# Performance work log

Hardware: AMD Instinct MI355X
Metric: run time of the kernel (lower is better)

## Reference

```python
import jax, jax.numpy as jnp
import numpy as np

B, HG, WG = 2, 64, 64
N = HG * WG
C_IN, C_HID, HEADS, C_OUT = 512, 256, 4, 512
NEG_SLOPE = 0.2   # PyG GATv2Conv default negative_slope
LN_EPS = 1e-5


def _grid_edges(h, w):
    """8-neighborhood grid graph, edge_index[0]=source, edge_index[1]=target."""
    nodes = np.arange(h * w).reshape(h, w)
    srcs, dsts = [], []
    for dh in (-1, 0, 1):
        for dw in (-1, 0, 1):
            if dh == 0 and dw == 0:
                continue
            r0, r1 = max(0, -dh), h - max(0, dh)
            c0, c1 = max(0, -dw), w - max(0, dw)
            srcs.append(nodes[r0:r1, c0:c1].ravel())
            dsts.append(nodes[r0 + dh:r1 + dh, c0 + dw:c1 + dw].ravel())
    return np.stack([np.concatenate(srcs), np.concatenate(dsts)]).astype(np.int64)


def setup_inputs() -> dict:
    key = jax.random.key(0)
    ks = iter(jax.random.split(key, 32))

    def p(shape, scale=0.02):
        return jax.random.normal(next(ks), shape, dtype=jnp.float32) * scale

    return {
        "rgb_features": jax.random.normal(next(ks), (B, N, C_IN), dtype=jnp.float32),
        "x_features": jax.random.normal(next(ks), (B, N, C_IN), dtype=jnp.float32),
        "edge_index": jnp.asarray(_grid_edges(HG, WG)),
        # modality_fusion: Linear(2*C_IN, C_HID) + LayerNorm
        "fusion_w": p((C_HID, 2 * C_IN)), "fusion_b": jnp.zeros((C_HID,), jnp.float32),
        "fusion_g": jnp.ones((C_HID,), jnp.float32), "fusion_beta": jnp.zeros((C_HID,), jnp.float32),
        # GATSegmentation.in_proj + norm
        "inproj_w": p((C_HID, C_HID)), "inproj_b": jnp.zeros((C_HID,), jnp.float32),
        "norm_g": jnp.ones((C_HID,), jnp.float32), "norm_b": jnp.zeros((C_HID,), jnp.float32),
        # GATv2Conv layer 0: C_HID -> C_HID, heads=4, concat=True
        "l0_wl": p((HEADS * C_HID, C_HID)), "l0_bl": jnp.zeros((HEADS * C_HID,), jnp.float32),
        "l0_wr": p((HEADS * C_HID, C_HID)), "l0_br": jnp.zeros((HEADS * C_HID,), jnp.float32),
        "l0_att": p((HEADS, C_HID)), "l0_bias": jnp.zeros((HEADS * C_HID,), jnp.float32),
        # GATv2Conv layer 1 (final): 4*C_HID -> C_HID, heads=1, concat=False
        "l1_wl": p((C_HID, HEADS * C_HID)), "l1_bl": jnp.zeros((C_HID,), jnp.float32),
        "l1_wr": p((C_HID, HEADS * C_HID)), "l1_br": jnp.zeros((C_HID,), jnp.float32),
        "l1_att": p((1, C_HID)), "l1_bias": jnp.zeros((C_HID,), jnp.float32),
        # final_proj: 1x1 conv C_HID -> C_OUT
        "fp_w": p((C_OUT, C_HID)), "fp_b": jnp.zeros((C_OUT,), jnp.float32),
    }


def _ln(x, g, b):
    mu = x.mean(-1, keepdims=True)
    v = ((x - mu) ** 2).mean(-1, keepdims=True)
    return (x - mu) * jax.lax.rsqrt(v + LN_EPS) * g + b


def _gatv2(x, src, dst, wl, bl, wr, br, att, bias, concat):
    """PyG GATv2Conv (share_weights=False): gather, leaky_relu logit, segment softmax over
    target neighborhoods, scatter-add aggregation."""
    n = x.shape[0]
    heads, c = att.shape
    xl = (x @ wl.T + bl).reshape(n, heads, c)   # source-side transform (x_j)
    xr = (x @ wr.T + br).reshape(n, heads, c)   # target-side transform (x_i)
    e = jax.nn.leaky_relu(xl[src] + xr[dst], NEG_SLOPE)        # [E, H, C]
    logit = jnp.einsum('ehc,hc->eh', e, att)                   # [E, H]
    m = jax.ops.segment_max(logit, dst, num_segments=n)
    p = jnp.exp(logit - m[dst])
    z = jax.ops.segment_sum(p, dst, num_segments=n)
    alpha = p / z[dst]                                          # softmax per target node
    out = jax.ops.segment_sum(xl[src] * alpha[..., None], dst, num_segments=n)  # [N, H, C]
    out = out.reshape(n, heads * c) if concat else out.mean(axis=1)
    return out + bias


def reference(rgb_features, x_features, edge_index, fusion_w, fusion_b, fusion_g, fusion_beta,
              inproj_w, inproj_b, norm_g, norm_b,
              l0_wl, l0_bl, l0_wr, l0_br, l0_att, l0_bias,
              l1_wl, l1_bl, l1_wr, l1_br, l1_att, l1_bias,
              fp_w, fp_b):
    b, n, _ = rgb_features.shape
    loops = jnp.arange(n, dtype=edge_index.dtype)  # PyG add_self_loops=True
    src = jnp.concatenate([edge_index[0], loops])
    dst = jnp.concatenate([edge_index[1], loops])

    def single(rgb, xm):  # one graph in the batch (original loops over B in Python)
        comb = jnp.concatenate([rgb, xm], axis=-1)                     # [N, 2*C_IN]
        f = jax.nn.relu(_ln(comb @ fusion_w.T + fusion_b, fusion_g, fusion_beta))
        h = jax.nn.relu(_ln(f @ inproj_w.T + inproj_b, norm_g, norm_b))
        h = jax.nn.relu(_gatv2(h, src, dst, l0_wl, l0_bl, l0_wr, l0_br, l0_att, l0_bias, True))
        h = jax.nn.relu(_gatv2(h, src, dst, l1_wl, l1_bl, l1_wr, l1_br, l1_att, l1_bias, False))
        return h                                                        # [N, C_HID]

    nodes = jax.vmap(single)(rgb_features, x_features)                  # [B, N, C_HID]
    img = nodes.reshape(b, HG, WG, C_HID)
    return jnp.einsum('bhwc,oc->bohw', img, fp_w) + fp_b[None, :, None, None]
```

## Files before the change

kernel.cpp:

```cpp
#include <hip/hip_runtime.h>


#define NNODE 4096
#define LN_EPS 1e-5f
#define LOG2E 1.4426950408889634f

typedef _Float16 half8 __attribute__((ext_vector_type(8)));
typedef _Float16 half4 __attribute__((ext_vector_type(4)));
typedef _Float16 h2 __attribute__((ext_vector_type(2)));
typedef float f32x4 __attribute__((ext_vector_type(4)));

__device__ __forceinline__ float wave_reduce_sum(float v) {
    #pragma unroll
    for (int off = 32; off > 0; off >>= 1) v += __shfl_xor(v, off, 64);
    return v;
}

__device__ __forceinline__ void gload_lds16(const void* g, void* l) {
    __builtin_amdgcn_global_load_lds(
        (const __attribute__((address_space(1))) void*)g,
        (__attribute__((address_space(3))) void*)l, 16, 0, 0);
}

template<int N> __device__ __forceinline__ void waitcnt_vm() {
    if constexpr (N <= 0)      asm volatile("s_waitcnt vmcnt(0)" ::: "memory");
    else if constexpr (N == 2) asm volatile("s_waitcnt vmcnt(2)" ::: "memory");
    else if constexpr (N == 3) asm volatile("s_waitcnt vmcnt(3)" ::: "memory");
    else if constexpr (N == 4) asm volatile("s_waitcnt vmcnt(4)" ::: "memory");
    else                       asm volatile("s_waitcnt vmcnt(8)" ::: "memory");
}
template<int N> __device__ __forceinline__ void waitcnt_vm_lgkm() {
    if constexpr (N <= 0)      asm volatile("s_waitcnt vmcnt(0) lgkmcnt(0)" ::: "memory");
    else if constexpr (N == 2) asm volatile("s_waitcnt vmcnt(2) lgkmcnt(0)" ::: "memory");
    else if constexpr (N == 3) asm volatile("s_waitcnt vmcnt(3) lgkmcnt(0)" ::: "memory");
    else                       asm volatile("s_waitcnt vmcnt(4) lgkmcnt(0)" ::: "memory");
}
__device__ __forceinline__ void barrier_raw() {
    asm volatile("s_barrier" ::: "memory");
}

__device__ __forceinline__ int xcd_swz(int lin, int total) {
    return (lin & 7) * (total >> 3) + (lin >> 3);
}

template<int IT, int JT, int OUTMODE>
__global__ __launch_bounds__(256) void gemm3_k(
    const _Float16* __restrict__ A, const _Float16* __restrict__ W,
    const float* __restrict__ bias_lo, const float* __restrict__ bias_hi,
    int nsplit, void* __restrict__ Cout, int K, int N)
{
    constexpr int BM = 32 * IT, BN = 32 * JT;
    constexpr int CA = (BM * 4) / 256;
    constexpr int CB = (BN * 4) / 256;
    constexpr int L = CA + CB;
    __shared__ _Float16 ldsA[3][BM * 32];
    __shared__ _Float16 ldsB[3][BN * 32];

    const int tid = threadIdx.x;
    const int lin = blockIdx.y * gridDim.x + blockIdx.x;
    const int swz = xcd_swz(lin, gridDim.x * gridDim.y);
    const int m0 = (swz / gridDim.x) * BM, n0 = (swz % gridDim.x) * BN;
    const int lane = tid & 63, w = tid >> 6;
    const int fr = lane & 15, kq = lane >> 4;
    const int sq = (kq ^ (fr & 3)) * 8;
    const int wm = (w & 1) * (16 * IT), wn = (w >> 1) * (16 * JT);

    const _Float16* aP[CA]; int aC[CA];
    #pragma unroll
    for (int i = 0; i < CA; ++i) {
        const int c = i * 256 + tid, r = c >> 2, q = (c & 3) ^ (r & 3);
        aP[i] = A + (size_t)(m0 + r) * K + q * 8;
        aC[i] = c * 8;
    }
    const _Float16* bP[CB]; int bC[CB];
    #pragma unroll
    for (int i = 0; i < CB; ++i) {
        const int c = i * 256 + tid, r = c >> 2, q = (c & 3) ^ (r & 3);
        bP[i] = W + (size_t)(n0 + r) * K + q * 8;
        bC[i] = c * 8;
    }

    f32x4 acc[IT][JT] = {};
    const int NT = K >> 5;

    #pragma unroll
    for (int i = 0; i < CA; ++i) gload_lds16(aP[i], &ldsA[0][aC[i]]);
    #pragma unroll
    for (int i = 0; i < CB; ++i) gload_lds16(bP[i], &ldsB[0][bC[i]]);
    #pragma unroll
    for (int i = 0; i < CA; ++i) gload_lds16(aP[i] + 32, &ldsA[1][aC[i]]);
    #pragma unroll
    for (int i = 0; i < CB; ++i) gload_lds16(bP[i] + 32, &ldsB[1][bC[i]]);

    int bi = 0;
    for (int t = 0; t < NT; ++t) {
        if (t + 1 < NT) waitcnt_vm<L>(); else waitcnt_vm<0>();
        barrier_raw();
        if (t + 2 < NT) {
            int nb = bi + 2; if (nb >= 3) nb -= 3;
            const int k2 = (t + 2) << 5;
            #pragma unroll
            for (int i = 0; i < CA; ++i) gload_lds16(aP[i] + k2, &ldsA[nb][aC[i]]);
            #pragma unroll
            for (int i = 0; i < CB; ++i) gload_lds16(bP[i] + k2, &ldsB[nb][bC[i]]);
        }
        half8 af[IT], bf[JT];
        #pragma unroll
        for (int i = 0; i < IT; ++i)
            af[i] = *(const half8*)&ldsA[bi][(wm + i * 16 + fr) * 32 + sq];
        #pragma unroll
        for (int j = 0; j < JT; ++j)
            bf[j] = *(const half8*)&ldsB[bi][(wn + j * 16 + fr) * 32 + sq];
        #pragma unroll
        for (int i = 0; i < IT; ++i)
            #pragma unroll
            for (int j = 0; j < JT; ++j) {
                if (OUTMODE == 1)
                    acc[i][j] = __builtin_amdgcn_mfma_f32_16x16x32_f16(
                        bf[j], af[i], acc[i][j], 0, 0, 0);
                else
                    acc[i][j] = __builtin_amdgcn_mfma_f32_16x16x32_f16(
                        af[i], bf[j], acc[i][j], 0, 0, 0);
            }
        ++bi; if (bi == 3) bi = 0;
    }

    if (OUTMODE == 1) {
        #pragma unroll
        for (int i = 0; i < IT; ++i) {
            const int m = m0 + wm + i * 16 + fr;
            #pragma unroll
            for (int j = 0; j < JT; ++j) {
                const int nb4 = n0 + wn + j * 16 + kq * 4;
                const float* bp = (nb4 < nsplit) ? bias_lo + nb4
                                                 : bias_hi + (nb4 - nsplit);
                const float4 bv = *(const float4*)bp;
                half4 ov = {(_Float16)(acc[i][j][0] + bv.x),
                            (_Float16)(acc[i][j][1] + bv.y),
                            (_Float16)(acc[i][j][2] + bv.z),
                            (_Float16)(acc[i][j][3] + bv.w)};
                *(half4*)((_Float16*)Cout + (size_t)m * N + nb4) = ov;
            }
        }
    } else {
        #pragma unroll
        for (int j = 0; j < JT; ++j) {
            const int col = n0 + wn + j * 16 + fr;
            const float bc = (col < nsplit) ? bias_lo[col] : bias_hi[col - nsplit];
            #pragma unroll
            for (int i = 0; i < IT; ++i) {
                const int mrun = m0 + wm + i * 16 + kq * 4;
                const int b = mrun >> 12, node = mrun & 4095;
                float4 ov = {acc[i][j][0] + bc, acc[i][j][1] + bc,
                             acc[i][j][2] + bc, acc[i][j][3] + bc};
                *(float4*)((float*)Cout + ((size_t)(b * N + col)) * 4096 + node) = ov;
            }
        }
    }
}

__global__ __launch_bounds__(512) void fusion2_k(
    const float* __restrict__ A0, const float* __restrict__ A1,
    const _Float16* __restrict__ W1, const float* __restrict__ b1,
    const float* __restrict__ g1, const float* __restrict__ be1,
    const _Float16* __restrict__ W2, const float* __restrict__ b2,
    const float* __restrict__ g2, const float* __restrict__ be2,
    _Float16* __restrict__ out)
{
    __shared__ _Float16 lA[3][32 * 32];
    __shared__ _Float16 lB[3][256 * 32];
    __shared__ float lC[32 * 260];
    __shared__ _Float16 lH[8 * 1024];

    const int tid = threadIdx.x;
    const int m0 = blockIdx.x * 32;
    const int lane = tid & 63, w = tid >> 6;
    const int fr = lane & 15, kq = lane >> 4;
    const int sq = (kq ^ (fr & 3)) * 8;
    const int wr = (w & 1) * 16, wc = (w >> 1) * 64;
    const bool stager = (tid < 128);

    const _Float16* bP[2]; int bC[2];
    #pragma unroll
    for (int i = 0; i < 2; ++i) {
        const int c = i * 512 + tid, r = c >> 2, q = (c & 3) ^ (r & 3);
        bP[i] = W1 + (size_t)r * 1024 + q * 8;
        bC[i] = c * 8;
    }
    const int ar = tid >> 2, aq = tid & 3;
    const int asw = (ar * 4 + (aq ^ (ar & 3))) * 8;
    float4 p0, p1;
    auto loadA = [&](int k) {
        const int gk = k + aq * 8;
        const float* s = (gk < 512) ? A0 + (size_t)(m0 + ar) * 512 + gk
                                    : A1 + (size_t)(m0 + ar) * 512 + gk - 512;
        p0 = *(const float4*)s;
        p1 = *(const float4*)(s + 4);
    };
    auto writeA = [&](int b) {
        half8 hv = {(_Float16)p0.x, (_Float16)p0.y, (_Float16)p0.z, (_Float16)p0.w,
                    (_Float16)p1.x, (_Float16)p1.y, (_Float16)p1.z, (_Float16)p1.w};
        *(half8*)&lA[b][asw] = hv;
    };

    f32x4 acc[4] = {};

    if (stager) { loadA(0); writeA(0); loadA(32); }
    #pragma unroll
    for (int i = 0; i < 2; ++i) gload_lds16(bP[i], &lB[0][bC[i]]);
    #pragma unroll
    for (int i = 0; i < 2; ++i) gload_lds16(bP[i] + 32, &lB[1][bC[i]]);

    int bi = 0;
    for (int t = 0; t < 32; ++t) {
        if (t + 1 < 32) {
            if (stager) waitcnt_vm_lgkm<4>(); else waitcnt_vm_lgkm<2>();
        } else {
            waitcnt_vm_lgkm<0>();
        }
        barrier_raw();
        int nb1 = bi + 1; if (nb1 >= 3) nb1 -= 3;
        int nb2 = bi + 2; if (nb2 >= 3) nb2 -= 3;
        if (stager && t + 1 < 32) writeA(nb1);
        if (t + 2 < 32) {
            const int k2 = (t + 2) << 5;
            if (stager) loadA(k2);
            #pragma unroll
            for (int i = 0; i < 2; ++i) gload_lds16(bP[i] + k2, &lB[nb2][bC[i]]);
        }
        half8 af = *(const half8*)&lA[bi][(wr + fr) * 32 + sq];
        half8 bf[4];
        #pragma unroll
        for (int j = 0; j < 4; ++j)
            bf[j] = *(const half8*)&lB[bi][(wc + j * 16 + fr) * 32 + sq];
        #pragma unroll
        for (int j = 0; j < 4; ++j)
            acc[j] = __builtin_amdgcn_mfma_f32_16x16x32_f16(af, bf[j], acc[j], 0, 0, 0);
        ++bi; if (bi == 3) bi = 0;
    }

    #pragma unroll
    for (int j = 0; j < 4; ++j) {
        const int col = wc + j * 16 + fr;
        const float bc = b1[col];
        #pragma unroll
        for (int r4 = 0; r4 < 4; ++r4)
            lC[(wr + kq * 4 + r4) * 260 + col] = acc[j][r4] + bc;
    }
    __syncthreads();

    {
        const float4 gv = *(const float4*)(g1 + lane * 4);
        const float4 bv = *(const float4*)(be1 + lane * 4);
        const int t2i = lane >> 3, gq = (lane >> 1) & 3, qo = (lane & 1) * 4;
        #pragma unroll
        for (int rr = 0; rr < 4; ++rr) {
            const int row = w * 4 + rr;
            const float4 v = *(const float4*)&lC[row * 260 + lane * 4];
            float s  = v.x + v.y + v.z + v.w;
            float s2 = v.x * v.x + v.y * v.y + v.z * v.z + v.w * v.w;
            s = wave_reduce_sum(s);
            s2 = wave_reduce_sum(s2);
            const float mu  = s * (1.0f / 256.0f);
            const float var = s2 * (1.0f / 256.0f) - mu * mu;
            const float rs  = rsqrtf(var + LN_EPS);
            half4 o;
            o[0] = (_Float16)fmaxf((v.x - mu) * rs * gv.x + bv.x, 0.f);
            o[1] = (_Float16)fmaxf((v.y - mu) * rs * gv.y + bv.y, 0.f);
            o[2] = (_Float16)fmaxf((v.z - mu) * rs * gv.z + bv.z, 0.f);
            o[3] = (_Float16)fmaxf((v.w - mu) * rs * gv.w + bv.w, 0.f);
            const int qslot = gq ^ (row & 3);
            *(half4*)&lH[t2i * 1024 + (row * 4 + qslot) * 8 + qo] = o;
        }
    }
    __syncthreads();

    const _Float16* b2P[2]; int b2C[2];
    #pragma unroll
    for (int i = 0; i < 2; ++i) {
        const int c = i * 512 + tid, r = c >> 2, q = (c & 3) ^ (r & 3);
        b2P[i] = W2 + (size_t)r * 256 + q * 8;
        b2C[i] = c * 8;
    }
    f32x4 acc2[4] = {};
    #pragma unroll
    for (int i = 0; i < 2; ++i) gload_lds16(b2P[i], &lB[0][b2C[i]]);
    #pragma unroll
    for (int i = 0; i < 2; ++i) gload_lds16(b2P[i] + 32, &lB[1][b2C[i]]);

    int bi2 = 0;
    for (int t2 = 0; t2 < 8; ++t2) {
        if (t2 + 1 < 8) waitcnt_vm<2>(); else waitcnt_vm<0>();
        barrier_raw();
        if (t2 + 2 < 8) {
            int nb = bi2 + 2; if (nb >= 3) nb -= 3;
            const int k2 = (t2 + 2) << 5;
            #pragma unroll
            for (int i = 0; i < 2; ++i) gload_lds16(b2P[i] + k2, &lB[nb][b2C[i]]);
        }
        const half8 af = *(const half8*)
            &lH[t2 * 1024 + ((wr + fr) * 4 + (kq ^ (fr & 3))) * 8];
        half8 bf[4];
        #pragma unroll
        for (int j = 0; j < 4; ++j)
            bf[j] = *(const half8*)&lB[bi2][(wc + j * 16 + fr) * 32 + sq];
        #pragma unroll
        for (int j = 0; j < 4; ++j)
            acc2[j] = __builtin_amdgcn_mfma_f32_16x16x32_f16(af, bf[j], acc2[j], 0, 0, 0);
        ++bi2; if (bi2 == 3) bi2 = 0;
    }

    #pragma unroll
    for (int j = 0; j < 4; ++j) {
        const int col = wc + j * 16 + fr;
        const float bc = b2[col];
        #pragma unroll
        for (int r4 = 0; r4 < 4; ++r4)
            lC[(wr + kq * 4 + r4) * 260 + col] = acc2[j][r4] + bc;
    }
    __syncthreads();

    {
        const float4 gv = *(const float4*)(g2 + lane * 4);
        const float4 bv = *(const float4*)(be2 + lane * 4);
        #pragma unroll
        for (int rr = 0; rr < 4; ++rr) {
            const int row = w * 4 + rr;
            const float4 v = *(const float4*)&lC[row * 260 + lane * 4];
            float s  = v.x + v.y + v.z + v.w;
            float s2 = v.x * v.x + v.y * v.y + v.z * v.z + v.w * v.w;
            s = wave_reduce_sum(s);
            s2 = wave_reduce_sum(s2);
            const float mu  = s * (1.0f / 256.0f);
            const float var = s2 * (1.0f / 256.0f) - mu * mu;
            const float rs  = rsqrtf(var + LN_EPS);
            half4 o;
            o[0] = (_Float16)fmaxf((v.x - mu) * rs * gv.x + bv.x, 0.f);
            o[1] = (_Float16)fmaxf((v.y - mu) * rs * gv.y + bv.y, 0.f);
            o[2] = (_Float16)fmaxf((v.z - mu) * rs * gv.z + bv.z, 0.f);
            o[3] = (_Float16)fmaxf((v.w - mu) * rs * gv.w + bv.w, 0.f);
            *(half4*)(out + (size_t)(m0 + row) * 256 + lane * 4) = o;
        }
    }
}

template<int HEADS, int LD, int XROFF, int OC>
__global__ __launch_bounds__(256) void gat4_k(
    const _Float16* __restrict__ xlr, const _Float16* __restrict__ att16,
    const float* __restrict__ bias, _Float16* __restrict__ out)
{
    const int tid = threadIdx.x, wv = tid >> 6, lane = tid & 63;
    const int g = lane >> 4, li = lane & 15;
    const int blk = xcd_swz(blockIdx.x, gridDim.x);
    const int wid = blk * 4 + wv;
    const int gi = (HEADS == 4) ? wid : wid * 4 + g;
    const int h  = (HEADS == 4) ? g : 0;
    const int node = gi & (NNODE - 1);
    const int base = gi - node;
    const int nr = node >> 6, nc = node & 63;
    const int co = h * 256 + li * 16;

    int sidx[9]; float msk[9];
    {
        const int drs[8] = {-1,-1,-1, 0, 0, 1, 1, 1};
        const int dcs[8] = {-1, 0, 1,-1, 1,-1, 0, 1};
        #pragma unroll
        for (int j = 0; j < 8; ++j) {
            const int rj = nr + drs[j], cj = nc + dcs[j];
            const bool v = ((unsigned)rj < 64u) & ((unsigned)cj < 64u);
            sidx[j] = v ? (rj * 64 + cj) : node;
            msk[j] = v ? 0.f : -1e30f;
        }
        sidx[8] = node; msk[8] = 0.f;
    }

    const _Float16* xp = xlr + (size_t)base * LD + co;

    half8 x0[9], x1[9];
    #pragma unroll
    for (int j = 0; j < 9; ++j) {
        x0[j] = *(const half8*)(xp + (size_t)sidx[j] * LD);
        x1[j] = *(const half8*)(xp + (size_t)sidx[j] * LD + 8);
    }
    const half8 xr0 = *(const half8*)(xlr + (size_t)gi * LD + XROFF + co);
    const half8 xr1 = *(const half8*)(xlr + (size_t)gi * LD + XROFF + co + 8);
    const half8 at0 = *(const half8*)(att16 + h * 256 + li * 16);
    const half8 at1 = *(const half8*)(att16 + h * 256 + li * 16 + 8);
    const h2 hz = {(_Float16)0.f, (_Float16)0.f};
    const h2 c02 = {(_Float16)0.2f, (_Float16)0.2f};

    float lg[9];
    #pragma unroll
    for (int j = 0; j < 9; ++j) {
        h2 p = hz;
        #pragma unroll
        for (int k = 0; k < 4; ++k) {
            h2 e = ((const h2*)&x0[j])[k] + ((const h2*)&xr0)[k];
            h2 tt = __builtin_elementwise_fma(
                __builtin_elementwise_min(e, hz), c02,
                __builtin_elementwise_max(e, hz));
            p = __builtin_elementwise_fma(tt, ((const h2*)&at0)[k], p);
        }
        #pragma unroll
        for (int k = 0; k < 4; ++k) {
            h2 e = ((const h2*)&x1[j])[k] + ((const h2*)&xr1)[k];
            h2 tt = __builtin_elementwise_fma(
                __builtin_elementwise_min(e, hz), c02,
                __builtin_elementwise_max(e, hz));
            p = __builtin_elementwise_fma(tt, ((const h2*)&at1)[k], p);
        }
        float pl = (float)p[0] + (float)p[1];
        pl += __shfl_xor(pl, 1, 64);
        pl += __shfl_xor(pl, 2, 64);
        pl += __shfl_xor(pl, 4, 64);
        pl += __shfl_xor(pl, 8, 64);
        lg[j] = pl + msk[j];
    }

    float m = lg[0];
    #pragma unroll
    for (int j = 1; j < 9; ++j) m = fmaxf(m, lg[j]);
    float pj[9], z = 0.f;
    #pragma unroll
    for (int j = 0; j < 9; ++j) { pj[j] = __builtin_amdgcn_exp2f(lg[j] - m); z += pj[j]; }
    const float inv = __builtin_amdgcn_rcpf(z);

    float acc[16];
    #pragma unroll
    for (int k = 0; k < 16; ++k) acc[k] = 0.f;
    #pragma unroll
    for (int j = 0; j < 9; ++j) {
        const float wj = pj[j];
        #pragma unroll
        for (int k = 0; k < 8; ++k) acc[k]     += wj * (float)x0[j][k];
        #pragma unroll
        for (int k = 0; k < 8; ++k) acc[8 + k] += wj * (float)x1[j][k];
    }
    float bv[16];
    #pragma unroll
    for (int q = 0; q < 4; ++q) {
        const float4 b4 = *(const float4*)(bias + h * 256 + li * 16 + q * 4);
        bv[q * 4 + 0] = b4.x; bv[q * 4 + 1] = b4.y;
        bv[q * 4 + 2] = b4.z; bv[q * 4 + 3] = b4.w;
    }
    half8 o0, o1;
    #pragma unroll
    for (int k = 0; k < 8; ++k) o0[k] = (_Float16)fmaxf(acc[k] * inv + bv[k], 0.f);
    #pragma unroll
    for (int k = 0; k < 8; ++k) o1[k] = (_Float16)fmaxf(acc[8 + k] * inv + bv[8 + k], 0.f);
    *(half8*)(out + (size_t)gi * OC + co) = o0;
    *(half8*)(out + (size_t)gi * OC + co + 8) = o1;
}

struct WTab {
    const float* src[9];
    int startblk[10];
    int nelem[9];
    int dstoff[9];
    float scale[9];
};

__global__ __launch_bounds__(256) void wconv_k(WTab t, _Float16* __restrict__ dst)
{
    const int b = blockIdx.x;
    int s = 0;
    #pragma unroll
    for (int i = 1; i < 9; ++i) s += (b >= t.startblk[i]);
    const int e0 = (b - t.startblk[s]) * 1024 + threadIdx.x * 4;
    if (e0 >= t.nelem[s]) return;
    const float4 v = *(const float4*)(t.src[s] + e0);
    const float sc = t.scale[s];
    half4 o = {(_Float16)(v.x * sc), (_Float16)(v.y * sc),
               (_Float16)(v.z * sc), (_Float16)(v.w * sc)};
    *(half4*)(dst + t.dstoff[s] + e0) = o;
}

extern "C" void kernel_launch(void* const* d_in, const int* in_sizes, int n_in,
                              void* d_out, int out_size, void* d_ws, size_t ws_size,
                              hipStream_t stream)
{
    const float* rgb       = (const float*)d_in[0];
    const float* xm        = (const float*)d_in[1];
    const float* fusion_w  = (const float*)d_in[3];
    const float* fusion_b  = (const float*)d_in[4];
    const float* fusion_g  = (const float*)d_in[5];
    const float* fusion_be = (const float*)d_in[6];
    const float* inproj_w  = (const float*)d_in[7];
    const float* inproj_b  = (const float*)d_in[8];
    const float* norm_g    = (const float*)d_in[9];
    const float* norm_b    = (const float*)d_in[10];
    const float* l0_wl     = (const float*)d_in[11];
    const float* l0_bl     = (const float*)d_in[12];
    const float* l0_wr     = (const float*)d_in[13];
    const float* l0_br     = (const float*)d_in[14];
    const float* l0_att    = (const float*)d_in[15];
    const float* l0_bias   = (const float*)d_in[16];
    const float* l1_wl     = (const float*)d_in[17];
    const float* l1_bl     = (const float*)d_in[18];
    const float* l1_wr     = (const float*)d_in[19];
    const float* l1_br     = (const float*)d_in[20];
    const float* l1_att    = (const float*)d_in[21];
    const float* l1_bias   = (const float*)d_in[22];
    const float* fp_w      = (const float*)d_in[23];
    const float* fp_b      = (const float*)d_in[24];

    char* ws = (char*)d_ws;
    _Float16* Wf16 = (_Float16*)ws;
    _Float16* H1   = (_Float16*)(ws + 4194304);
    _Float16* XLR0 = (_Float16*)(ws + 8388608);
    _Float16* GO0  = (_Float16*)(ws + 41943040);
    _Float16* XLR1 = (_Float16*)(ws + 58720256);
    _Float16* GO1  = (_Float16*)(ws + 67108864);

    _Float16* w_fus  = Wf16 + 0;
    _Float16* w_inp  = Wf16 + 262144;
    _Float16* w_l0   = Wf16 + 327680;
    _Float16* w_l1   = Wf16 + 851968;
    _Float16* w_fp   = Wf16 + 1376256;
    _Float16* att0_h = Wf16 + 1507328;
    _Float16* att1_h = Wf16 + 1508352;

    WTab t;
    const float* srcs[9] = {fusion_w, inproj_w, l0_wl, l0_wr, l1_wl, l1_wr,
                            fp_w, l0_att, l1_att};
    const int nel[9]  = {262144, 65536, 262144, 262144, 262144, 262144,
                         131072, 1024, 256};
    const int doff[9] = {0, 262144, 327680, 589824, 851968, 1114112,
                         1376256, 1507328, 1508352};
    const int sblk[10] = {0, 256, 320, 576, 832, 1088, 1344, 1472, 1473, 1474};
    for (int i = 0; i < 9; ++i) {
        t.src[i] = srcs[i]; t.nelem[i] = nel[i]; t.dstoff[i] = doff[i];
        t.scale[i] = (i >= 7) ? LOG2E : 1.0f;
    }
    for (int i = 0; i < 10; ++i) t.startblk[i] = sblk[i];

    wconv_k<<<1474, 256, 0, stream>>>(t, Wf16);

    fusion2_k<<<256, 512, 0, stream>>>(
        rgb, xm, w_fus, fusion_b, fusion_g, fusion_be,
        w_inp, inproj_b, norm_g, norm_b, H1);

    gemm3_k<4, 4, 1><<<dim3(16, 64), 256, 0, stream>>>(
        H1, w_l0, l0_bl, l0_br, 1024, XLR0, 256, 2048);

    gat4_k<4, 2048, 1024, 1024><<<2048, 256, 0, stream>>>(
        XLR0, att0_h, l0_bias, GO0);

    gemm3_k<2, 4, 1><<<dim3(4, 128), 256, 0, stream>>>(
        GO0, w_l1, l1_bl, l1_br, 256, XLR1, 1024, 512);

    gat4_k<1, 512, 256, 256><<<512, 256, 0, stream>>>(
        XLR1, att1_h, l1_bias, GO1);

    gemm3_k<2, 4, 2><<<dim3(4, 128), 256, 0, stream>>>(
        GO1, w_fp, fp_b, fp_b, 512, d_out, 256, 512);
}
```

Measured before the change: 116.8 us.

## Halve fusion2 row tile to 16 and use double-buffered pipeline

Fused fusion+inproj kernel now processes 16 rows per block instead of 32, doubling the grid to 512 blocks so more CUs are occupied. Each wave covers 32 output columns instead of a 16x64 sub-tile. The triple-buffered, counter-based pipeline is replaced by a simpler double buffer that waits on vmcnt(0) and a full __syncthreads each K step. The weight tiles are now reloaded by twice as many blocks, and the per-step full wait lets less load latency overlap with compute.

```diff
diff --git a/kernel.cpp b/kernel.cpp
--- a/kernel.cpp
+++ b/kernel.cpp
@@ -28,12 +28,6 @@
     else if constexpr (N == 3) asm volatile("s_waitcnt vmcnt(3)" ::: "memory");
     else if constexpr (N == 4) asm volatile("s_waitcnt vmcnt(4)" ::: "memory");
     else                       asm volatile("s_waitcnt vmcnt(8)" ::: "memory");
-}
-template<int N> __device__ __forceinline__ void waitcnt_vm_lgkm() {
-    if constexpr (N <= 0)      asm volatile("s_waitcnt vmcnt(0) lgkmcnt(0)" ::: "memory");
-    else if constexpr (N == 2) asm volatile("s_waitcnt vmcnt(2) lgkmcnt(0)" ::: "memory");
-    else if constexpr (N == 3) asm volatile("s_waitcnt vmcnt(3) lgkmcnt(0)" ::: "memory");
-    else                       asm volatile("s_waitcnt vmcnt(4) lgkmcnt(0)" ::: "memory");
 }
 __device__ __forceinline__ void barrier_raw() {
     asm volatile("s_barrier" ::: "memory");
@@ -167,18 +161,18 @@
     const float* __restrict__ g2, const float* __restrict__ be2,
     _Float16* __restrict__ out)
 {
-    __shared__ _Float16 lA[3][32 * 32];
-    __shared__ _Float16 lB[3][256 * 32];
-    __shared__ float lC[32 * 260];
-    __shared__ _Float16 lH[8 * 1024];
+    __shared__ _Float16 lA[2][16 * 32];
+    __shared__ _Float16 lB[2][256 * 32];
+    __shared__ float lC[16 * 260];
+    __shared__ _Float16 lH[8 * 512];
 
     const int tid = threadIdx.x;
-    const int m0 = blockIdx.x * 32;
+    const int m0 = blockIdx.x * 16;
     const int lane = tid & 63, w = tid >> 6;
     const int fr = lane & 15, kq = lane >> 4;
     const int sq = (kq ^ (fr & 3)) * 8;
-    const int wr = (w & 1) * 16, wc = (w >> 1) * 64;
-    const bool stager = (tid < 128);
+    const int wc = w * 32;
+    const bool stager = (tid < 64);
 
     const _Float16* bP[2]; int bC[2];
     #pragma unroll
@@ -203,49 +197,46 @@
         *(half8*)&lA[b][asw] = hv;
     };
 
-    f32x4 acc[4] = {};
-
-    if (stager) { loadA(0); writeA(0); loadA(32); }
+    f32x4 acc[2] = {};
+
+    if (stager) { loadA(0); writeA(0); }
     #pragma unroll
     for (int i = 0; i < 2; ++i) gload_lds16(bP[i], &lB[0][bC[i]]);
-    #pragma unroll
-    for (int i = 0; i < 2; ++i) gload_lds16(bP[i] + 32, &lB[1][bC[i]]);
-
-    int bi = 0;
+    asm volatile("s_waitcnt vmcnt(0)" ::: "memory");
+    __syncthreads();
+
+    int cur = 0;
     for (int t = 0; t < 32; ++t) {
-        if (t + 1 < 32) {
-            if (stager) waitcnt_vm_lgkm<4>(); else waitcnt_vm_lgkm<2>();
-        } else {
-            waitcnt_vm_lgkm<0>();
-        }
-        barrier_raw();
-        int nb1 = bi + 1; if (nb1 >= 3) nb1 -= 3;
-        int nb2 = bi + 2; if (nb2 >= 3) nb2 -= 3;
-        if (stager && t + 1 < 32) writeA(nb1);
-        if (t + 2 < 32) {
-            const int k2 = (t + 2) << 5;
-            if (stager) loadA(k2);
-            #pragma unroll
-            for (int i = 0; i < 2; ++i) gload_lds16(bP[i] + k2, &lB[nb2][bC[i]]);
-        }
-        half8 af = *(const half8*)&lA[bi][(wr + fr) * 32 + sq];
-        half8 bf[4];
-        #pragma unroll
-        for (int j = 0; j < 4; ++j)
-            bf[j] = *(const half8*)&lB[bi][(wc + j * 16 + fr) * 32 + sq];
-        #pragma unroll
-        for (int j = 0; j < 4; ++j)
+        const int pf = (t + 1 < 32);
+        if (pf) {
+            const int k1 = (t + 1) << 5;
+            if (stager) loadA(k1);
+            #pragma unroll
+            for (int i = 0; i < 2; ++i) gload_lds16(bP[i] + k1, &lB[cur ^ 1][bC[i]]);
+        }
+        const half8 af = *(const half8*)&lA[cur][fr * 32 + sq];
+        half8 bf[2];
+        #pragma unroll
+        for (int j = 0; j < 2; ++j)
+            bf[j] = *(const half8*)&lB[cur][(wc + j * 16 + fr) * 32 + sq];
+        #pragma unroll
+        for (int j = 0; j < 2; ++j)
             acc[j] = __builtin_amdgcn_mfma_f32_16x16x32_f16(af, bf[j], acc[j], 0, 0, 0);
-        ++bi; if (bi == 3) bi = 0;
-    }
-
-    #pragma unroll
-    for (int j = 0; j < 4; ++j) {
+        if (pf) {
+            if (stager) writeA(cur ^ 1);
+            asm volatile("s_waitcnt vmcnt(0)" ::: "memory");
+            __syncthreads();
+            cur ^= 1;
+        }
+    }
+
+    #pragma unroll
+    for (int j = 0; j < 2; ++j) {
         const int col = wc + j * 16 + fr;
         const float bc = b1[col];
         #pragma unroll
         for (int r4 = 0; r4 < 4; ++r4)
-            lC[(wr + kq * 4 + r4) * 260 + col] = acc[j][r4] + bc;
+            lC[(kq * 4 + r4) * 260 + col] = acc[j][r4] + bc;
     }
     __syncthreads();
 
@@ -254,8 +245,8 @@
         const float4 bv = *(const float4*)(be1 + lane * 4);
         const int t2i = lane >> 3, gq = (lane >> 1) & 3, qo = (lane & 1) * 4;
         #pragma unroll
-        for (int rr = 0; rr < 4; ++rr) {
-            const int row = w * 4 + rr;
+        for (int rr = 0; rr < 2; ++rr) {
+            const int row = w * 2 + rr;
             const float4 v = *(const float4*)&lC[row * 260 + lane * 4];
             float s  = v.x + v.y + v.z + v.w;
             float s2 = v.x * v.x + v.y * v.y + v.z * v.z + v.w * v.w;
@@ -270,7 +261,7 @@
             o[2] = (_Float16)fmaxf((v.z - mu) * rs * gv.z + bv.z, 0.f);
             o[3] = (_Float16)fmaxf((v.w - mu) * rs * gv.w + bv.w, 0.f);
             const int qslot = gq ^ (row & 3);
-            *(half4*)&lH[t2i * 1024 + (row * 4 + qslot) * 8 + qo] = o;
+            *(half4*)&lH[t2i * 512 + (row * 4 + qslot) * 8 + qo] = o;
         }
     }
     __syncthreads();
@@ -282,41 +273,44 @@
         b2P[i] = W2 + (size_t)r * 256 + q * 8;
         b2C[i] = c * 8;
     }
-    f32x4 acc2[4] = {};
+    f32x4 acc2[2] = {};
     #pragma unroll
     for (int i = 0; i < 2; ++i) gload_lds16(b2P[i], &lB[0][b2C[i]]);
-    #pragma unroll
-    for (int i = 0; i < 2; ++i) gload_lds16(b2P[i] + 32, &lB[1][b2C[i]]);
-
-    int bi2 = 0;
+    asm volatile("s_waitcnt vmcnt(0)" ::: "memory");
+    __syncthreads();
+
+    int cur2 = 0;
     for (int t2 = 0; t2 < 8; ++t2) {
-        if (t2 + 1 < 8) waitcnt_vm<2>(); else waitcnt_vm<0>();
-        barrier_raw();
-        if (t2 + 2 < 8) {
-            int nb = bi2 + 2; if (nb >= 3) nb -= 3;
-            const int k2 = (t2 + 2) << 5;
-            #pragma unroll
-            for (int i = 0; i < 2; ++i) gload_lds16(b2P[i] + k2, &lB[nb][b2C[i]]);
+        const int pf = (t2 + 1 < 8);
+        if (pf) {
+            const int k1 = (t2 + 1) << 5;
+            #pragma unroll
+            for (int i = 0; i < 2; ++i) gload_lds16(b2P[i] + k1, &lB[cur2 ^ 1][b2C[i]]);
         }
         const half8 af = *(const half8*)
-            &lH[t2 * 1024 + ((wr + fr) * 4 + (kq ^ (fr & 3))) * 8];
-        half8 bf[4];
-        #pragma unroll
-        for (int j = 0; j < 4; ++j)
-            bf[j] = *(const half8*)&lB[bi2][(wc + j * 16 + fr) * 32 + sq];
-        #pragma unroll
-        for (int j = 0; j < 4; ++j)
+            &lH[t2 * 512 + (fr * 4 + (kq ^ (fr & 3))) * 8];
+        half8 bf[2];
+        #pragma unroll
+        for (int j = 0; j < 2; ++j)
+            bf[j] = *(const half8*)&lB[cur2][(wc + j * 16 + fr) * 32 + sq];
+        #pragma unroll
+        for (int j = 0; j < 2; ++j)
             acc2[j] = __builtin_amdgcn_mfma_f32_16x16x32_f16(af, bf[j], acc2[j], 0, 0, 0);
-        ++bi2; if (bi2 == 3) bi2 = 0;
-    }
-
-    #pragma unroll
-    for (int j = 0; j < 4; ++j) {
+        if (pf) {
+            asm volatile("s_waitcnt vmcnt(0)" ::: "memory");
+            __syncthreads();
+            cur2 ^= 1;
+        }
+    }
+
+    __syncthreads();
+    #pragma unroll
+    for (int j = 0; j < 2; ++j) {
         const int col = wc + j * 16 + fr;
         const float bc = b2[col];
         #pragma unroll
         for (int r4 = 0; r4 < 4; ++r4)
-            lC[(wr + kq * 4 + r4) * 260 + col] = acc2[j][r4] + bc;
+            lC[(kq * 4 + r4) * 260 + col] = acc2[j][r4] + bc;
     }
     __syncthreads();
 
@@ -324,8 +318,8 @@
         const float4 gv = *(const float4*)(g2 + lane * 4);
         const float4 bv = *(const float4*)(be2 + lane * 4);
         #pragma unroll
-        for (int rr = 0; rr < 4; ++rr) {
-            const int row = w * 4 + rr;
+        for (int rr = 0; rr < 2; ++rr) {
+            const int row = w * 2 + rr;
             const float4 v = *(const float4*)&lC[row * 260 + lane * 4];
             float s  = v.x + v.y + v.z + v.w;
             float s2 = v.x * v.x + v.y * v.y + v.z * v.z + v.w * v.w;
@@ -536,7 +530,7 @@
 
     wconv_k<<<1474, 256, 0, stream>>>(t, Wf16);
 
-    fusion2_k<<<256, 512, 0, stream>>>(
+    fusion2_k<<<512, 512, 0, stream>>>(
         rgb, xm, w_fus, fusion_b, fusion_g, fusion_be,
         w_inp, inproj_b, norm_g, norm_b, H1);
 
```

New measurement: 117.4 us. Within noise of the previous version (+0.6%).
